# Optimization experiments

Hardware: AMD Instinct MI355X
Metric: run time of the kernel (lower is better)

## Reference

```python
import jax, jax.numpy as jnp
import numpy as np

B, S, D = 2, 2048, 1024
H, DH = 16, 64  # num_head, head_dim; H*DH == D


def setup_inputs() -> dict:
    key = jax.random.key(0)
    ks = jax.random.split(key, 10)
    stdv = 1.0 / np.sqrt(D)
    def lin(k):
        kw, kb = jax.random.split(k)
        W = jax.random.uniform(kw, (D, D), jnp.float32, -stdv, stdv)
        b = jax.random.uniform(kb, (D,), jnp.float32, -stdv, stdv)
        return W, b
    Wq, bq = lin(ks[0]); Wk, bk = lin(ks[1]); Wv, bv = lin(ks[2]); Wo, bo = lin(ks[3])
    x = jax.random.normal(ks[4], (B, S, D), jnp.float32)
    # causal mask: True = attend
    mask = jnp.tril(jnp.ones((S, S), jnp.bool_))
    mask = jnp.broadcast_to(mask, (B, S, S))
    return {"x": x, "mask": mask, "Wq": Wq, "bq": bq, "Wk": Wk, "bk": bk,
            "Wv": Wv, "bv": bv, "Wo": Wo, "bo": bo}


def _split_head(t):
    # [B,S,D] -> [B*H, S, DH]
    return t.reshape(B, S, H, DH).transpose(0, 2, 1, 3).reshape(B * H, S, DH)


def _concat_head(t):
    # [B*H, S, DH] -> [B, S, D]
    return t.reshape(B, H, S, DH).transpose(0, 2, 1, 3).reshape(B, S, D)


def reference(x, mask, Wq, bq, Wk, bk, Wv, bv, Wo, bo):
    q = _split_head(x @ Wq.T + bq)
    k = _split_head(x @ Wk.T + bk)
    v = _split_head(x @ Wv.T + bv)
    scale = 1.0 / jnp.sqrt(jnp.float32(DH))
    # scores: [B, H, S, S], masked softmax (flash-attention math, unfused ref)
    scores = jnp.einsum('nqd,nkd->nqk', q, k).reshape(B, H, S, S) * scale
    scores = jnp.where(mask[:, None, :, :], scores, jnp.finfo(scores.dtype).min)
    attn = jax.nn.softmax(scores, axis=-1)
    out = jnp.einsum('bhqk,nkd->bhqd', attn, v.reshape(B, H, S, DH).reshape(B * H, S, DH)).reshape(B * H, S, DH) if False else jnp.einsum('nqk,nkd->nqd', attn.reshape(B * H, S, S), v)
    return _concat_head(out) @ Wo.T + bo
```

## Files before the change

kernel.cpp:

```cpp
#include <hip/hip_runtime.h>
#include <cstdint>

#define S_LEN  2048
#define NH     16
#define DHEAD  64
#define DMODEL 1024

typedef __bf16 bf16x8 __attribute__((ext_vector_type(8)));
typedef float  f32x4  __attribute__((ext_vector_type(4)));

__device__ __forceinline__ unsigned short f2bf(float x) {
  union { float f; unsigned int u; } c; c.f = x;
  unsigned int u = c.u;
  return (unsigned short)((u + 0x7fffu + ((u >> 16) & 1u)) >> 16);
}

__device__ __forceinline__ void glds16(const void* g, void* l) {
  __builtin_amdgcn_global_load_lds(
      (const __attribute__((address_space(1))) void*)g,
      (__attribute__((address_space(3))) void*)l, 16, 0, 0);
}

__device__ __forceinline__ f32x4 mfma16(bf16x8 a, bf16x8 b, f32x4 c) {
  return __builtin_amdgcn_mfma_f32_16x16x32_bf16(a, b, c, 0, 0, 0);
}

__global__ void cvt_all(const float* __restrict__ x,
                        const float* __restrict__ Wq,
                        const float* __restrict__ Wk,
                        const float* __restrict__ Wv,
                        const float* __restrict__ Wo,
                        unsigned short* __restrict__ xb,
                        unsigned short* __restrict__ wqkv,
                        unsigned short* __restrict__ wo) {
  const int b = blockIdx.x;
  const float* src;
  unsigned short* dst;
  int off;
  if (b < 4096)      { src = x;  dst = xb;                off = b; }
  else if (b < 5120) { src = Wq; dst = wqkv;              off = b - 4096; }
  else if (b < 6144) { src = Wk; dst = wqkv + (1 << 20);  off = b - 5120; }
  else if (b < 7168) { src = Wv; dst = wqkv + (2 << 20);  off = b - 6144; }
  else               { src = Wo; dst = wo;                off = b - 7168; }
  const int i = (off * 256 + threadIdx.x) * 4;
  float4 v = *(const float4*)&src[i];
  ushort4 r;
  r.x = f2bf(v.x); r.y = f2bf(v.y); r.z = f2bf(v.z); r.w = f2bf(v.w);
  *(ushort4*)&dst[i] = r;
}

template<int MODE>
__global__ __launch_bounds__(256)
void gemm_bt(const unsigned short* __restrict__ A,
             const unsigned short* __restrict__ W,
             const float* __restrict__ bias0,
             const float* __restrict__ bias1,
             const float* __restrict__ bias2,
             unsigned short* __restrict__ Qb,
             unsigned short* __restrict__ Kb,
             unsigned short* __restrict__ Vt,
             float* __restrict__ Out,
             int K) {
  __shared__ __align__(16) unsigned short As[128 * 32];
  __shared__ __align__(16) unsigned short Bs[128 * 32];
  const int t    = threadIdx.x;
  const int lane = t & 63;
  const int w    = t >> 6;
  const int lr   = lane & 15, lq = lane >> 4;
  const int wm   = (w >> 1) * 64, wn = (w & 1) * 64;
  const int m0   = blockIdx.y * 128, n0 = blockIdx.x * 128;
  const int ra   = t >> 2, ca = (t & 3) * 8;

  f32x4 acc[4][4] = {};

  const int kt = K >> 5;
  for (int kk = 0; kk < kt; ++kk) {
    const int k0 = kk << 5;
    glds16(A + (m0 + ra) * K + k0 + ca,      &As[ra * 32 + ca]);
    glds16(A + (m0 + 64 + ra) * K + k0 + ca, &As[(64 + ra) * 32 + ca]);
    glds16(W + (n0 + ra) * K + k0 + ca,      &Bs[ra * 32 + ca]);
    glds16(W + (n0 + 64 + ra) * K + k0 + ca, &Bs[(64 + ra) * 32 + ca]);
    __syncthreads();
    bf16x8 af[4], bg[4];
#pragma unroll
    for (int i = 0; i < 4; ++i)
      af[i] = *(const bf16x8*)&As[(wm + i * 16 + lr) * 32 + lq * 8];
#pragma unroll
    for (int j = 0; j < 4; ++j)
      bg[j] = *(const bf16x8*)&Bs[(wn + j * 16 + lr) * 32 + lq * 8];
#pragma unroll
    for (int i = 0; i < 4; ++i)
#pragma unroll
      for (int j = 0; j < 4; ++j)
        acc[i][j] = mfma16(af[i], bg[j], acc[i][j]);
    __syncthreads();
  }

#pragma unroll
  for (int i = 0; i < 4; ++i) {
#pragma unroll
    for (int j = 0; j < 4; ++j) {
#pragma unroll
      for (int r = 0; r < 4; ++r) {
        const int m = m0 + wm + i * 16 + lq * 4 + r;
        const int n = n0 + wn + j * 16 + lr;
        float v = acc[i][j][r];
        if (MODE == 0) {
          const int tsel = n >> 10, d = n & 1023;
          const float* bp = (tsel == 0) ? bias0 : ((tsel == 1) ? bias1 : bias2);
          v += bp[d];
          const int bidx = m >> 11, s = m & (S_LEN - 1);
          const int h = d >> 6, dh = d & 63;
          const int bh = bidx * NH + h;
          if (tsel == 0) {
            v *= 0.125f * 1.44269504088896f;
            Qb[(bh * S_LEN + s) * DHEAD + dh] = f2bf(v);
          } else if (tsel == 1) {
            Kb[(bh * S_LEN + s) * DHEAD + dh] = f2bf(v);
          } else {
            Vt[(bh * DHEAD + dh) * S_LEN + s] = f2bf(v);
          }
        } else {
          v += bias0[n];
          Out[m * DMODEL + n] = v;
        }
      }
    }
  }
}

__global__ __launch_bounds__(256, 3)
void flash_kernel(const unsigned short* __restrict__ Qb,
                  const unsigned short* __restrict__ Kb,
                  const unsigned short* __restrict__ Vt,
                  unsigned short* __restrict__ Ocat) {
  __shared__ __align__(16) unsigned short Ks[2][2][64 * 32];
  __shared__ __align__(16) unsigned short Vs[2][2][64 * 32];
  __shared__ __align__(16) unsigned short pls[4][16 * 76];
  const int w = threadIdx.x >> 6, lane = threadIdx.x & 63;
  const int lr = lane & 15, lq = lane >> 4;
  const int bh = blockIdx.x;
  const int sb = 31 - blockIdx.y;
  const char* Kc = (const char*)(Kb + bh * (S_LEN * DHEAD));
  const char* Vc = (const char*)(Vt + bh * (DHEAD * S_LEN));
  const unsigned short* Qp = Qb + bh * (S_LEN * DHEAD);
  const int bb = bh >> 4, h = bh & 15;
  unsigned short* pw = &pls[w][0];

  const int hh  = w & 1;
  const int rbb = (w >> 1) * 2;
  const int rlane = lane >> 2;
  const int clane = (lane & 3) * 16;

  const int q0 = sb * 64 + w * 16;
  const bf16x8 qlo = *(const bf16x8*)&Qp[(q0 + lr) * DHEAD + lq * 8];
  const bf16x8 qhi = *(const bf16x8*)&Qp[(q0 + lr) * DHEAD + 32 + lq * 8];

  bf16x8 ones;
#pragma unroll
  for (int j = 0; j < 8; ++j) ones[j] = (__bf16)1.0f;

  f32x4 o[4] = {};
  f32x4 lacc = {};
  float mrow = -1e30f;
  const int nfull = sb;

  auto stage = [&](int buf, int sk0) {
#pragma unroll
    for (int j = 0; j < 2; ++j) {
      const int rb = rbb + j;
      glds16(Kc + (sk0 + rb * 16 + rlane) * 128 + hh * 64 + clane,
             &Ks[buf][hh][rb * 16 * 32]);
      glds16(Vc + (rb * 16 + rlane) * 4096 + (sk0 + hh * 32) * 2 + clane,
             &Vs[buf][hh][rb * 16 * 32]);
    }
  };

  stage(0, 0);
  for (int kt = 0; kt <= nfull; ++kt) {
    const int buf = kt & 1;
    __syncthreads();
    if (kt < nfull) stage(1 - buf, (kt + 1) << 6);

    f32x4 st[4] = {};
    const unsigned short* Kl = Ks[buf][0];
    const unsigned short* Kh = Ks[buf][1];
#pragma unroll
    for (int t = 0; t < 4; ++t) {
      st[t] = mfma16(*(const bf16x8*)&Kl[(t * 16 + lr) * 32 + lq * 8], qlo, st[t]);
      st[t] = mfma16(*(const bf16x8*)&Kh[(t * 16 + lr) * 32 + lq * 8], qhi, st[t]);
    }
    float p[4][4];
    if (kt == nfull) {
      const int q = q0 + lr, sk0 = kt << 6;
#pragma unroll
      for (int t = 0; t < 4; ++t)
#pragma unroll
        for (int r = 0; r < 4; ++r) {
          const int k = sk0 + t * 16 + lq * 4 + r;
          p[t][r] = (k <= q) ? st[t][r] : -1e30f;
        }
    } else {
#pragma unroll
      for (int t = 0; t < 4; ++t)
#pragma unroll
        for (int r = 0; r < 4; ++r) p[t][r] = st[t][r];
    }
    float mx = p[0][0];
#pragma unroll
    for (int t = 0; t < 4; ++t)
#pragma unroll
      for (int r = 0; r < 4; ++r) mx = fmaxf(mx, p[t][r]);
    mx = fmaxf(mx, __shfl_xor(mx, 16));
    mx = fmaxf(mx, __shfl_xor(mx, 32));
    const float nm = fmaxf(mrow, mx);
    const float alpha = __builtin_amdgcn_exp2f(mrow - nm);
    mrow = nm;
#pragma unroll
    for (int t = 0; t < 4; ++t)
#pragma unroll
      for (int r = 0; r < 4; ++r)
        p[t][r] = __builtin_amdgcn_exp2f(p[t][r] - nm);
#pragma unroll
    for (int tt = 0; tt < 4; ++tt) o[tt] *= alpha;
    lacc *= alpha;

#pragma unroll
    for (int t = 0; t < 4; ++t) {
      ushort4 pk;
      pk.x = f2bf(p[t][0]); pk.y = f2bf(p[t][1]);
      pk.z = f2bf(p[t][2]); pk.w = f2bf(p[t][3]);
      *(ushort4*)&pw[lr * 76 + t * 16 + lq * 4] = pk;
    }
    const bf16x8 pf0 = *(const bf16x8*)&pw[lr * 76 + lq * 8];
    const bf16x8 pf1 = *(const bf16x8*)&pw[lr * 76 + 32 + lq * 8];
    const unsigned short* Vl = Vs[buf][0];
    const unsigned short* Vh = Vs[buf][1];
#pragma unroll
    for (int tt = 0; tt < 4; ++tt) {
      o[tt] = mfma16(*(const bf16x8*)&Vl[(tt * 16 + lr) * 32 + lq * 8], pf0, o[tt]);
      o[tt] = mfma16(*(const bf16x8*)&Vh[(tt * 16 + lr) * 32 + lq * 8], pf1, o[tt]);
    }
    lacc = mfma16(ones, pf0, lacc);
    lacc = mfma16(ones, pf1, lacc);
  }

  const float inv = 1.f / lacc[0];
#pragma unroll
  for (int tt = 0; tt < 4; ++tt) {
    ushort4 ov;
    ov.x = f2bf(o[tt][0] * inv); ov.y = f2bf(o[tt][1] * inv);
    ov.z = f2bf(o[tt][2] * inv); ov.w = f2bf(o[tt][3] * inv);
    *(ushort4*)&Ocat[(bb * S_LEN + q0 + lr) * DMODEL + h * DHEAD + tt * 16 + lq * 4] = ov;
  }
}

extern "C" void kernel_launch(void* const* d_in, const int* in_sizes, int n_in,
                              void* d_out, int out_size, void* d_ws, size_t ws_size,
                              hipStream_t stream) {
  const float* x  = (const float*)d_in[0];
  const float* Wq = (const float*)d_in[2];
  const float* bq = (const float*)d_in[3];
  const float* Wk = (const float*)d_in[4];
  const float* bk = (const float*)d_in[5];
  const float* Wv = (const float*)d_in[6];
  const float* bv = (const float*)d_in[7];
  const float* Wo = (const float*)d_in[8];
  const float* bo = (const float*)d_in[9];
  float* out = (float*)d_out;

  char* ws = (char*)d_ws;
  unsigned short* xb   = (unsigned short*)(ws);
  unsigned short* wqkv = (unsigned short*)(ws + (8ull  << 20));
  unsigned short* wo   = (unsigned short*)(ws + (14ull << 20));
  unsigned short* Qb   = (unsigned short*)(ws + (16ull << 20));
  unsigned short* Kb   = (unsigned short*)(ws + (24ull << 20));
  unsigned short* Vt   = (unsigned short*)(ws + (32ull << 20));
  unsigned short* Ocat = (unsigned short*)(ws + (40ull << 20));

  cvt_all<<<8192, 256, 0, stream>>>(x, Wq, Wk, Wv, Wo, xb, wqkv, wo);

  gemm_bt<0><<<dim3(24, 32), 256, 0, stream>>>(xb, wqkv, bq, bk, bv,
                                               Qb, Kb, Vt, nullptr, 1024);
  flash_kernel<<<dim3(32, 32), 256, 0, stream>>>(Qb, Kb, Vt, Ocat);
  gemm_bt<1><<<dim3(8, 32), 256, 0, stream>>>(Ocat, wo, bo, nullptr, nullptr,
                                              nullptr, nullptr, nullptr, out, 1024);
}
```

Measured before the change: 232.1 us.

## Use packed bf16 conversions, swizzle P tile, retile output GEMM, raise flash occupancy

Replaces the manual float-to-bf16 rounding with the hardware packed conversion builtin when it is available, in the weight conversion, flash output and GEMM epilogues. The QKV epilogue hoists the tensor select per block and writes V transposed as packed 4-element stores. The flash kernel's per-wave P staging buffer uses an XOR swizzle instead of padding to avoid LDS bank conflicts, and its launch bounds ask for 4 blocks per SM. The output projection GEMM uses 128x64 tiles to launch more blocks. These aim to cut ALU conversion cost, LDS conflicts and underutilization, at the risk of register spills from the higher occupancy target.

```diff
diff --git a/kernel.cpp b/kernel.cpp
--- a/kernel.cpp
+++ b/kernel.cpp
@@ -7,12 +7,32 @@
 #define DMODEL 1024
 
 typedef __bf16 bf16x8 __attribute__((ext_vector_type(8)));
+typedef __bf16 bf16x2 __attribute__((ext_vector_type(2)));
 typedef float  f32x4  __attribute__((ext_vector_type(4)));
 
 __device__ __forceinline__ unsigned short f2bf(float x) {
   union { float f; unsigned int u; } c; c.f = x;
   unsigned int u = c.u;
   return (unsigned short)((u + 0x7fffu + ((u >> 16) & 1u)) >> 16);
+}
+
+__device__ __forceinline__ unsigned int pkbf(float a, float b) {
+#if __has_builtin(__builtin_amdgcn_cvt_pk_bf16_f32)
+  bf16x2 r = __builtin_amdgcn_cvt_pk_bf16_f32(a, b);
+  return *(unsigned int*)&r;
+#else
+  return (unsigned int)f2bf(a) | ((unsigned int)f2bf(b) << 16);
+#endif
+}
+
+__device__ __forceinline__ unsigned short f2bf1(float x) {
+#if __has_builtin(__builtin_amdgcn_cvt_pk_bf16_f32)
+  bf16x2 r = __builtin_amdgcn_cvt_pk_bf16_f32(x, x);
+  union { bf16x2 v; unsigned int u; } c; c.v = r;
+  return (unsigned short)(c.u & 0xffffu);
+#else
+  return f2bf(x);
+#endif
 }
 
 __device__ __forceinline__ void glds16(const void* g, void* l) {
@@ -44,12 +64,13 @@
   else               { src = Wo; dst = wo;                off = b - 7168; }
   const int i = (off * 256 + threadIdx.x) * 4;
   float4 v = *(const float4*)&src[i];
-  ushort4 r;
-  r.x = f2bf(v.x); r.y = f2bf(v.y); r.z = f2bf(v.z); r.w = f2bf(v.w);
-  *(ushort4*)&dst[i] = r;
-}
-
-template<int MODE>
+  uint2 r;
+  r.x = pkbf(v.x, v.y);
+  r.y = pkbf(v.z, v.w);
+  *(uint2*)&dst[i] = r;
+}
+
+template<int MODE, int BN>
 __global__ __launch_bounds__(256)
 void gemm_bt(const unsigned short* __restrict__ A,
              const unsigned short* __restrict__ W,
@@ -61,17 +82,18 @@
              unsigned short* __restrict__ Vt,
              float* __restrict__ Out,
              int K) {
+  constexpr int JN = BN / 32;
   __shared__ __align__(16) unsigned short As[128 * 32];
-  __shared__ __align__(16) unsigned short Bs[128 * 32];
+  __shared__ __align__(16) unsigned short Bs[BN * 32];
   const int t    = threadIdx.x;
   const int lane = t & 63;
   const int w    = t >> 6;
   const int lr   = lane & 15, lq = lane >> 4;
-  const int wm   = (w >> 1) * 64, wn = (w & 1) * 64;
-  const int m0   = blockIdx.y * 128, n0 = blockIdx.x * 128;
+  const int wm   = (w >> 1) * 64, wn = (w & 1) * (BN / 2);
+  const int m0   = blockIdx.y * 128, n0 = blockIdx.x * BN;
   const int ra   = t >> 2, ca = (t & 3) * 8;
 
-  f32x4 acc[4][4] = {};
+  f32x4 acc[4][JN] = {};
 
   const int kt = K >> 5;
   for (int kk = 0; kk < kt; ++kk) {
@@ -79,64 +101,77 @@
     glds16(A + (m0 + ra) * K + k0 + ca,      &As[ra * 32 + ca]);
     glds16(A + (m0 + 64 + ra) * K + k0 + ca, &As[(64 + ra) * 32 + ca]);
     glds16(W + (n0 + ra) * K + k0 + ca,      &Bs[ra * 32 + ca]);
-    glds16(W + (n0 + 64 + ra) * K + k0 + ca, &Bs[(64 + ra) * 32 + ca]);
+    if (BN == 128)
+      glds16(W + (n0 + 64 + ra) * K + k0 + ca, &Bs[(64 + ra) * 32 + ca]);
     __syncthreads();
-    bf16x8 af[4], bg[4];
+    bf16x8 af[4], bg[JN];
 #pragma unroll
     for (int i = 0; i < 4; ++i)
       af[i] = *(const bf16x8*)&As[(wm + i * 16 + lr) * 32 + lq * 8];
 #pragma unroll
-    for (int j = 0; j < 4; ++j)
+    for (int j = 0; j < JN; ++j)
       bg[j] = *(const bf16x8*)&Bs[(wn + j * 16 + lr) * 32 + lq * 8];
 #pragma unroll
     for (int i = 0; i < 4; ++i)
 #pragma unroll
-      for (int j = 0; j < 4; ++j)
+      for (int j = 0; j < JN; ++j)
         acc[i][j] = mfma16(af[i], bg[j], acc[i][j]);
     __syncthreads();
   }
 
-#pragma unroll
-  for (int i = 0; i < 4; ++i) {
-#pragma unroll
-    for (int j = 0; j < 4; ++j) {
-#pragma unroll
-      for (int r = 0; r < 4; ++r) {
-        const int m = m0 + wm + i * 16 + lq * 4 + r;
-        const int n = n0 + wn + j * 16 + lr;
-        float v = acc[i][j][r];
-        if (MODE == 0) {
-          const int tsel = n >> 10, d = n & 1023;
-          const float* bp = (tsel == 0) ? bias0 : ((tsel == 1) ? bias1 : bias2);
-          v += bp[d];
-          const int bidx = m >> 11, s = m & (S_LEN - 1);
-          const int h = d >> 6, dh = d & 63;
-          const int bh = bidx * NH + h;
-          if (tsel == 0) {
-            v *= 0.125f * 1.44269504088896f;
-            Qb[(bh * S_LEN + s) * DHEAD + dh] = f2bf(v);
-          } else if (tsel == 1) {
-            Kb[(bh * S_LEN + s) * DHEAD + dh] = f2bf(v);
-          } else {
-            Vt[(bh * DHEAD + dh) * S_LEN + s] = f2bf(v);
+  if (MODE == 0) {
+    const int tsel = n0 >> 10;
+#pragma unroll
+    for (int i = 0; i < 4; ++i) {
+#pragma unroll
+      for (int j = 0; j < JN; ++j) {
+        const int mb = m0 + wm + i * 16 + lq * 4;
+        const int n  = n0 + wn + j * 16 + lr;
+        const int d  = n & 1023;
+        const int bidx = mb >> 11, s = mb & (S_LEN - 1);
+        const int h = d >> 6, dh = d & 63;
+        const int bh = bidx * NH + h;
+        const float bv0 = (tsel == 0) ? bias0[d] : ((tsel == 1) ? bias1[d] : bias2[d]);
+        if (tsel == 2) {
+          uint2 pv;
+          pv.x = pkbf(acc[i][j][0] + bv0, acc[i][j][1] + bv0);
+          pv.y = pkbf(acc[i][j][2] + bv0, acc[i][j][3] + bv0);
+          *(uint2*)&Vt[(bh * DHEAD + dh) * S_LEN + s] = pv;
+        } else if (tsel == 0) {
+#pragma unroll
+          for (int r = 0; r < 4; ++r) {
+            float v = (acc[i][j][r] + bv0) * (0.125f * 1.44269504088896f);
+            Qb[(bh * S_LEN + s + r) * DHEAD + dh] = f2bf1(v);
           }
         } else {
-          v += bias0[n];
-          Out[m * DMODEL + n] = v;
+#pragma unroll
+          for (int r = 0; r < 4; ++r)
+            Kb[(bh * S_LEN + s + r) * DHEAD + dh] = f2bf1(acc[i][j][r] + bv0);
         }
       }
     }
+  } else {
+#pragma unroll
+    for (int i = 0; i < 4; ++i)
+#pragma unroll
+      for (int j = 0; j < JN; ++j)
+#pragma unroll
+        for (int r = 0; r < 4; ++r) {
+          const int m = m0 + wm + i * 16 + lq * 4 + r;
+          const int n = n0 + wn + j * 16 + lr;
+          Out[m * DMODEL + n] = acc[i][j][r] + bias0[n];
+        }
   }
 }
 
-__global__ __launch_bounds__(256, 3)
+__global__ __launch_bounds__(256, 4)
 void flash_kernel(const unsigned short* __restrict__ Qb,
                   const unsigned short* __restrict__ Kb,
                   const unsigned short* __restrict__ Vt,
                   unsigned short* __restrict__ Ocat) {
   __shared__ __align__(16) unsigned short Ks[2][2][64 * 32];
   __shared__ __align__(16) unsigned short Vs[2][2][64 * 32];
-  __shared__ __align__(16) unsigned short pls[4][16 * 76];
+  __shared__ __align__(16) unsigned short pls[4][1024];
   const int w = threadIdx.x >> 6, lane = threadIdx.x & 63;
   const int lr = lane & 15, lq = lane >> 4;
   const int bh = blockIdx.x;
@@ -146,6 +181,7 @@
   const unsigned short* Qp = Qb + bh * (S_LEN * DHEAD);
   const int bb = bh >> 4, h = bh & 15;
   unsigned short* pw = &pls[w][0];
+  const int swz = lr & 7;
 
   const int hh  = w & 1;
   const int rbb = (w >> 1) * 2;
@@ -227,13 +263,14 @@
 
 #pragma unroll
     for (int t = 0; t < 4; ++t) {
-      ushort4 pk;
-      pk.x = f2bf(p[t][0]); pk.y = f2bf(p[t][1]);
-      pk.z = f2bf(p[t][2]); pk.w = f2bf(p[t][3]);
-      *(ushort4*)&pw[lr * 76 + t * 16 + lq * 4] = pk;
-    }
-    const bf16x8 pf0 = *(const bf16x8*)&pw[lr * 76 + lq * 8];
-    const bf16x8 pf1 = *(const bf16x8*)&pw[lr * 76 + 32 + lq * 8];
+      uint2 pk;
+      pk.x = pkbf(p[t][0], p[t][1]);
+      pk.y = pkbf(p[t][2], p[t][3]);
+      const int g = t * 2 + (lq >> 1);
+      *(uint2*)&pw[lr * 64 + ((g ^ swz) << 3) + ((lq & 1) << 2)] = pk;
+    }
+    const bf16x8 pf0 = *(const bf16x8*)&pw[lr * 64 + ((lq ^ swz) << 3)];
+    const bf16x8 pf1 = *(const bf16x8*)&pw[lr * 64 + (((4 + lq) ^ swz) << 3)];
     const unsigned short* Vl = Vs[buf][0];
     const unsigned short* Vh = Vs[buf][1];
 #pragma unroll
@@ -248,10 +285,10 @@
   const float inv = 1.f / lacc[0];
 #pragma unroll
   for (int tt = 0; tt < 4; ++tt) {
-    ushort4 ov;
-    ov.x = f2bf(o[tt][0] * inv); ov.y = f2bf(o[tt][1] * inv);
-    ov.z = f2bf(o[tt][2] * inv); ov.w = f2bf(o[tt][3] * inv);
-    *(ushort4*)&Ocat[(bb * S_LEN + q0 + lr) * DMODEL + h * DHEAD + tt * 16 + lq * 4] = ov;
+    uint2 ov;
+    ov.x = pkbf(o[tt][0] * inv, o[tt][1] * inv);
+    ov.y = pkbf(o[tt][2] * inv, o[tt][3] * inv);
+    *(uint2*)&Ocat[(bb * S_LEN + q0 + lr) * DMODEL + h * DHEAD + tt * 16 + lq * 4] = ov;
   }
 }
 
@@ -280,9 +317,9 @@
 
   cvt_all<<<8192, 256, 0, stream>>>(x, Wq, Wk, Wv, Wo, xb, wqkv, wo);
 
-  gemm_bt<0><<<dim3(24, 32), 256, 0, stream>>>(xb, wqkv, bq, bk, bv,
-                                               Qb, Kb, Vt, nullptr, 1024);
+  gemm_bt<0, 128><<<dim3(24, 32), 256, 0, stream>>>(xb, wqkv, bq, bk, bv,
+                                                    Qb, Kb, Vt, nullptr, 1024);
   flash_kernel<<<dim3(32, 32), 256, 0, stream>>>(Qb, Kb, Vt, Ocat);
-  gemm_bt<1><<<dim3(8, 32), 256, 0, stream>>>(Ocat, wo, bo, nullptr, nullptr,
-                                              nullptr, nullptr, nullptr, out, 1024);
-}
+  gemm_bt<1, 64><<<dim3(16, 32), 256, 0, stream>>>(Ocat, wo, bo, nullptr, nullptr,
+                                                   nullptr, nullptr, nullptr, out, 1024);
+}
```

Result: faster. 211.1 us (-9.1%).
